# Kernel tuning notes

Hardware: AMD Instinct MI355X
Metric: run time of the kernel (lower is better)

## Reference

```python
import jax, jax.numpy as jnp
import numpy as np

HEADS = 8


def setup_inputs() -> dict:
    key = jax.random.key(0)
    k1, k2, k3, k4, k5, k6 = jax.random.split(key, 6)
    B, S, E = 2, 2048, 512
    D = E // HEADS
    return {
        "values": jax.random.normal(k1, (B, S, E), dtype=jnp.float32),
        "keys": jax.random.normal(k2, (B, S, E), dtype=jnp.float32),
        "queries": jax.random.normal(k3, (B, S, E), dtype=jnp.float32),
        "mask": jax.random.randint(k4, (B, 1, 1, S), 0, 2, dtype=jnp.int32),
        "W_v": jax.random.normal(k5, (D, D), dtype=jnp.float32) * (1.0 / np.sqrt(D)),
        "W_o": jax.random.normal(k6, (E, E), dtype=jnp.float32) * (1.0 / np.sqrt(E)),
        "b_o": jnp.zeros((E,), dtype=jnp.float32),
    }


def reference(values, keys, queries, mask, W_v, W_o, b_o):
    B, S, E = queries.shape
    H = HEADS
    D = E // H
    # reshape to (b, s, h, d) and apply the SAME W_v linear to v, k, q
    # (faithful to the original, which calls self.values on all three)
    v = jnp.einsum('bshd,ed->bshe', values.reshape(B, -1, H, D), W_v)
    k = jnp.einsum('bshd,ed->bshe', keys.reshape(B, -1, H, D), W_v)
    q = jnp.einsum('bshd,ed->bshe', queries.reshape(B, -1, H, D), W_v)
    # unscaled attention scores (original has no 1/sqrt(d))
    energy = jnp.einsum('bqhd,bkhd->bhqk', q, k)  # (b, h, q, k)
    energy = jnp.where(mask == 0, -jnp.inf, energy)
    attn = jax.nn.softmax(energy, axis=3)
    out = jnp.einsum('bhqk,bkhd->bqhd', attn, v)  # (b, q, h, d)
    out = out.reshape(B, S, E)
    return out @ W_o.T + b_o
```

## Files before the change

kernel.cpp:

```cpp
#include <hip/hip_runtime.h>


#define B_ 2
#define S_ 2048
#define E_ 512
#define H_ 8
#define D_ 64

#define LOG2E 1.4426950408889634f
#define KEEP_BIAS (-92.332483f)

typedef unsigned short ushort_t;
typedef __attribute__((ext_vector_type(8))) short short8;
typedef __attribute__((ext_vector_type(8))) _Float16 half8;
typedef __attribute__((ext_vector_type(4))) float f32x4;

__device__ __forceinline__ ushort_t f2bs(float x) {
    union { float f; unsigned int u; } a; a.f = x;
    unsigned int u = a.u;
    u += 0x7fffu + ((u >> 16) & 1u);
    return (ushort_t)(u >> 16);
}
__device__ __forceinline__ float bs2f(ushort_t h) {
    union { unsigned int u; float f; } a; a.u = ((unsigned int)h) << 16;
    return a.f;
}
__device__ __forceinline__ ushort_t f2hs(float x) {
    _Float16 h = (_Float16)x;
    ushort_t u; __builtin_memcpy(&u, &h, 2);
    return u;
}
__device__ __forceinline__ void split16(const float4* g, ushort_t* hi, ushort_t* lo) {
    #pragma unroll
    for (int q = 0; q < 4; ++q) {
        float4 f = g[q];
        float vv[4] = {f.x, f.y, f.z, f.w};
        #pragma unroll
        for (int j = 0; j < 4; ++j) {
            ushort_t h = f2bs(vv[j]);
            hi[q * 4 + j] = h;
            lo[q * 4 + j] = f2bs(vv[j] - bs2f(h));
        }
    }
}

__global__ void __launch_bounds__(256) proj_mfma(
    const float* __restrict__ quer, const float* __restrict__ keys,
    const float* __restrict__ vals, const float* __restrict__ Wv,
    const float* __restrict__ Wo,
    ushort_t* __restrict__ qf, ushort_t* __restrict__ kf,
    ushort_t* __restrict__ vt, ushort_t* __restrict__ Wob)
{
    __shared__ ushort_t Ah[64 * 72], Al[64 * 72];
    __shared__ ushort_t Bh[64 * 72], Bl[64 * 72];
    const int tens = blockIdx.y;
    const int bx = blockIdx.x;
    const int t = threadIdx.x;

    if (tens == 3) {
        if (bx < 128) {
            int g = (bx * 256 + t) * 8;
            float4 f0 = *(const float4*)(Wo + g);
            float4 f1 = *(const float4*)(Wo + g + 4);
            ushort_t tmp[8] = {f2bs(f0.x), f2bs(f0.y), f2bs(f0.z), f2bs(f0.w),
                               f2bs(f1.x), f2bs(f1.y), f2bs(f1.z), f2bs(f1.w)};
            *(uint4*)&Wob[g] = *(uint4*)tmp;
        }
        return;
    }

    const float* src = tens == 0 ? quer : (tens == 1 ? keys : vals);
    const int st = bx & 31, bh = bx >> 5;
    const int b = bh >> 3, h = bh & 7;
    const int s0 = st * 64;

    {
        int e = t >> 2, dg = (t & 3) * 16;
        ushort_t th[16], tl[16];
        split16((const float4*)(Wv + e * 64 + dg), th, tl);
        *(uint4*)&Bh[e * 72 + dg] = *(uint4*)th;  *(uint4*)&Bh[e * 72 + dg + 8] = *(uint4*)(th + 8);
        *(uint4*)&Bl[e * 72 + dg] = *(uint4*)tl;  *(uint4*)&Bl[e * 72 + dg + 8] = *(uint4*)(tl + 8);
    }
    {
        int row = t >> 2, cg = (t & 3) * 16;
        const float* g = src + ((size_t)b * S_ + s0 + row) * 512 + h * 64 + cg;
        ushort_t th[16], tl[16];
        split16((const float4*)g, th, tl);
        *(uint4*)&Ah[row * 72 + cg] = *(uint4*)th;  *(uint4*)&Ah[row * 72 + cg + 8] = *(uint4*)(th + 8);
        *(uint4*)&Al[row * 72 + cg] = *(uint4*)tl;  *(uint4*)&Al[row * 72 + cg + 8] = *(uint4*)(tl + 8);
    }
    __syncthreads();

    const int w = t >> 6, lm = t & 15, quad = (t >> 4) & 3;
    f32x4 acc[4];
    #pragma unroll
    for (int nt = 0; nt < 4; ++nt) acc[nt] = (f32x4){0.f, 0.f, 0.f, 0.f};

    __builtin_amdgcn_s_setprio(1);
    #pragma unroll
    for (int kk = 0; kk < 2; ++kk) {
        short8 ah = *(const short8*)&Ah[(w * 16 + lm) * 72 + kk * 32 + quad * 8];
        short8 al = *(const short8*)&Al[(w * 16 + lm) * 72 + kk * 32 + quad * 8];
        #pragma unroll
        for (int nt = 0; nt < 4; ++nt) {
            short8 bh8 = *(const short8*)&Bh[(nt * 16 + lm) * 72 + kk * 32 + quad * 8];
            short8 bl8 = *(const short8*)&Bl[(nt * 16 + lm) * 72 + kk * 32 + quad * 8];
            acc[nt] = __builtin_amdgcn_mfma_f32_16x16x32_bf16(ah, bh8, acc[nt], 0, 0, 0);
            acc[nt] = __builtin_amdgcn_mfma_f32_16x16x32_bf16(al, bh8, acc[nt], 0, 0, 0);
            acc[nt] = __builtin_amdgcn_mfma_f32_16x16x32_bf16(ah, bl8, acc[nt], 0, 0, 0);
        }
    }
    __builtin_amdgcn_s_setprio(0);

    if (tens < 2) {
        ushort_t* dst = tens == 0 ? qf : kf;
        const float sc = tens == 0 ? LOG2E : 1.0f;
        #pragma unroll
        for (int nt = 0; nt < 4; ++nt) {
            #pragma unroll
            for (int r = 0; r < 4; ++r) {
                size_t addr = ((size_t)bh * S_ + s0 + w * 16 + quad * 4 + r) * 64 + nt * 16 + lm;
                dst[addr] = f2hs(acc[nt][r] * sc);
            }
        }
    } else {
        #pragma unroll
        for (int nt = 0; nt < 4; ++nt) {
            unsigned int p0 = (unsigned int)f2bs(acc[nt][0]) | ((unsigned int)f2bs(acc[nt][1]) << 16);
            unsigned int p1 = (unsigned int)f2bs(acc[nt][2]) | ((unsigned int)f2bs(acc[nt][3]) << 16);
            uint2 pk; pk.x = p0; pk.y = p1;
            size_t addr = ((size_t)bh * 64 + nt * 16 + lm) * S_ + s0 + w * 16 + quad * 4;
            *(uint2*)&vt[addr] = pk;
        }
    }
}

__global__ void __launch_bounds__(512, 2) attn_mfma(
    const ushort_t* __restrict__ qf, const ushort_t* __restrict__ kf,
    const ushort_t* __restrict__ vt, const int* __restrict__ mask,
    ushort_t* __restrict__ ctx)
{
    __shared__ ushort_t Ks[4][64 * 72];
    __shared__ ushort_t Vt[4][64 * 72];
    __shared__ ushort_t Ps[8][32 * 72];
    __shared__ float    mb[4][64];

    const int bx0 = blockIdx.x;
    const int bx = (bx0 & 7) * 64 + (bx0 >> 3);
    const int qt = bx & 31;
    const int bh = bx >> 5;
    const int b  = bh >> 3;
    const int t  = threadIdx.x;
    const int w  = t >> 6;
    const int wq = w & 1;
    const int ws = w >> 1;
    const int lm = t & 15, quad = (t >> 4) & 3;
    const int lane = t & 63;
    const int q0 = qt * 64;

    const int stile = w & 3;
    const bool isV = w >= 4;
    const size_t kstage0 = ((size_t)bh * S_ + stile * 64 + lane) * 64;
    const size_t vstage0 = ((size_t)bh * 64 + lane) * S_ + stile * 64;
    ushort_t* sdst = isV ? &Vt[stile][lane * 72] : &Ks[stile][lane * 72];
    const ushort_t* sgl = isV ? vt : kf;
    const size_t sg0 = isV ? vstage0 : kstage0;
    const size_t sgstep = isV ? 256 : 16384;

    half8 aq00, aq01, aq10, aq11;
    {
        size_t qr0 = ((size_t)bh * S_ + q0 + wq * 32 + lm) * 64 + quad * 8;
        size_t qr1 = ((size_t)bh * S_ + q0 + wq * 32 + 16 + lm) * 64 + quad * 8;
        aq00 = *(const half8*)&qf[qr0];
        aq01 = *(const half8*)&qf[qr0 + 32];
        aq10 = *(const half8*)&qf[qr1];
        aq11 = *(const half8*)&qf[qr1 + 32];
    }
    short8 ones;
    #pragma unroll
    for (int j = 0; j < 8; ++j) ones[j] = (short)0x3F80;

    f32x4 acc[2][4];
    f32x4 accl[2];
    #pragma unroll
    for (int qg = 0; qg < 2; ++qg) {
        accl[qg] = (f32x4){0.f, 0.f, 0.f, 0.f};
        #pragma unroll
        for (int nt = 0; nt < 4; ++nt) acc[qg][nt] = (f32x4){0.f, 0.f, 0.f, 0.f};
    }

    {
        uint4 p0 = *(const uint4*)&sgl[sg0];
        uint4 p1 = *(const uint4*)&sgl[sg0 + 8];
        uint4 p2 = *(const uint4*)&sgl[sg0 + 16];
        uint4 p3 = *(const uint4*)&sgl[sg0 + 24];
        uint4 p4 = *(const uint4*)&sgl[sg0 + 32];
        uint4 p5 = *(const uint4*)&sgl[sg0 + 40];
        uint4 p6 = *(const uint4*)&sgl[sg0 + 48];
        uint4 p7 = *(const uint4*)&sgl[sg0 + 56];
        *(uint4*)&sdst[0]  = p0;  *(uint4*)&sdst[8]  = p1;
        *(uint4*)&sdst[16] = p2;  *(uint4*)&sdst[24] = p3;
        *(uint4*)&sdst[32] = p4;  *(uint4*)&sdst[40] = p5;
        *(uint4*)&sdst[48] = p6;  *(uint4*)&sdst[56] = p7;
        if (t < 256) mb[t >> 6][t & 63] = mask[b * S_ + t] ? KEEP_BIAS : -1e30f;
    }
    __syncthreads();

    for (int is = 0; is < 8; ++is) {
        const bool pf = is < 7;

        uint4 s0r, s1r, s2r, s3r, s4r, s5r, s6r, s7r; int mnx = 0;
        if (pf) {
            size_t g = sg0 + (size_t)(is + 1) * sgstep;
            s0r = *(const uint4*)&sgl[g];
            s1r = *(const uint4*)&sgl[g + 8];
            s2r = *(const uint4*)&sgl[g + 16];
            s3r = *(const uint4*)&sgl[g + 24];
            s4r = *(const uint4*)&sgl[g + 32];
            s5r = *(const uint4*)&sgl[g + 40];
            s6r = *(const uint4*)&sgl[g + 48];
            s7r = *(const uint4*)&sgl[g + 56];
            if (t < 256) mnx = mask[b * S_ + (is + 1) * 256 + t];
        }

        const ushort_t* Kc = Ks[ws];
        const ushort_t* Vc = Vt[ws];

        #pragma unroll
        for (int nt = 0; nt < 4; ++nt) {
            f32x4 binit = *(const f32x4*)&mb[ws][nt * 16 + quad * 4];
            f32x4 s0v = binit, s1v = binit;
            __builtin_amdgcn_s_setprio(1);
            #pragma unroll
            for (int kk = 0; kk < 2; ++kk) {
                half8 ak = *(const half8*)&Kc[(nt * 16 + lm) * 72 + kk * 32 + quad * 8];
                half8 aqa = kk ? aq01 : aq00;
                half8 aqb = kk ? aq11 : aq10;
                s0v = __builtin_amdgcn_mfma_f32_16x16x32_f16(ak, aqa, s0v, 0, 0, 0);
                s1v = __builtin_amdgcn_mfma_f32_16x16x32_f16(ak, aqb, s1v, 0, 0, 0);
            }
            __builtin_amdgcn_s_setprio(0);
            uint2 p0d, p1d;
            p0d.x = (unsigned int)f2bs(__builtin_amdgcn_exp2f(s0v[0])) |
                    ((unsigned int)f2bs(__builtin_amdgcn_exp2f(s0v[1])) << 16);
            p0d.y = (unsigned int)f2bs(__builtin_amdgcn_exp2f(s0v[2])) |
                    ((unsigned int)f2bs(__builtin_amdgcn_exp2f(s0v[3])) << 16);
            p1d.x = (unsigned int)f2bs(__builtin_amdgcn_exp2f(s1v[0])) |
                    ((unsigned int)f2bs(__builtin_amdgcn_exp2f(s1v[1])) << 16);
            p1d.y = (unsigned int)f2bs(__builtin_amdgcn_exp2f(s1v[2])) |
                    ((unsigned int)f2bs(__builtin_amdgcn_exp2f(s1v[3])) << 16);
            *(uint2*)&Ps[w][(lm) * 72 + nt * 16 + quad * 4]      = p0d;
            *(uint2*)&Ps[w][(16 + lm) * 72 + nt * 16 + quad * 4] = p1d;
        }

        __builtin_amdgcn_s_setprio(1);
        #pragma unroll
        for (int kk = 0; kk < 2; ++kk) {
            short8 ap0 = *(const short8*)&Ps[w][(lm) * 72 + kk * 32 + quad * 8];
            short8 ap1 = *(const short8*)&Ps[w][(16 + lm) * 72 + kk * 32 + quad * 8];
            #pragma unroll
            for (int nt = 0; nt < 4; ++nt) {
                short8 bv = *(const short8*)&Vc[(nt * 16 + lm) * 72 + kk * 32 + quad * 8];
                acc[0][nt] = __builtin_amdgcn_mfma_f32_16x16x32_bf16(ap0, bv, acc[0][nt], 0, 0, 0);
                acc[1][nt] = __builtin_amdgcn_mfma_f32_16x16x32_bf16(ap1, bv, acc[1][nt], 0, 0, 0);
            }
            accl[0] = __builtin_amdgcn_mfma_f32_16x16x32_bf16(ap0, ones, accl[0], 0, 0, 0);
            accl[1] = __builtin_amdgcn_mfma_f32_16x16x32_bf16(ap1, ones, accl[1], 0, 0, 0);
        }
        __builtin_amdgcn_s_setprio(0);

        __syncthreads();
        if (pf) {
            *(uint4*)&sdst[0]  = s0r;  *(uint4*)&sdst[8]  = s1r;
            *(uint4*)&sdst[16] = s2r;  *(uint4*)&sdst[24] = s3r;
            *(uint4*)&sdst[32] = s4r;  *(uint4*)&sdst[40] = s5r;
            *(uint4*)&sdst[48] = s6r;  *(uint4*)&sdst[56] = s7r;
            if (t < 256) mb[t >> 6][t & 63] = mnx ? KEEP_BIAS : -1e30f;
            __syncthreads();
        }
    }

    float* cfO = (float*)Ks;
    float* cfL = (float*)Vt;
    __syncthreads();
    if (ws & 1) {
        const int wid = wq * 2 + (ws >> 1);
        #pragma unroll
        for (int qg = 0; qg < 2; ++qg) {
            const int bO = ((wid * 2 + qg) * 64 + lane) * 17;
            #pragma unroll
            for (int nt = 0; nt < 4; ++nt)
                #pragma unroll
                for (int r = 0; r < 4; ++r) cfO[bO + nt * 4 + r] = acc[qg][nt][r];
            const int bL = ((wid * 2 + qg) * 64 + lane) * 5;
            #pragma unroll
            for (int r = 0; r < 4; ++r) cfL[bL + r] = accl[qg][r];
        }
    }
    __syncthreads();
    if (!(ws & 1)) {
        const int wid = wq * 2 + (ws >> 1);
        #pragma unroll
        for (int qg = 0; qg < 2; ++qg) {
            const int bO = ((wid * 2 + qg) * 64 + lane) * 17;
            #pragma unroll
            for (int nt = 0; nt < 4; ++nt)
                #pragma unroll
                for (int r = 0; r < 4; ++r) acc[qg][nt][r] += cfO[bO + nt * 4 + r];
            const int bL = ((wid * 2 + qg) * 64 + lane) * 5;
            #pragma unroll
            for (int r = 0; r < 4; ++r) accl[qg][r] += cfL[bL + r];
        }
    }
    __syncthreads();
    if (ws == 2) {
        #pragma unroll
        for (int qg = 0; qg < 2; ++qg) {
            const int bO = ((wq * 2 + qg) * 64 + lane) * 17;
            #pragma unroll
            for (int nt = 0; nt < 4; ++nt)
                #pragma unroll
                for (int r = 0; r < 4; ++r) cfO[bO + nt * 4 + r] = acc[qg][nt][r];
            const int bL = ((wq * 2 + qg) * 64 + lane) * 5;
            #pragma unroll
            for (int r = 0; r < 4; ++r) cfL[bL + r] = accl[qg][r];
        }
    }
    __syncthreads();
    if (ws == 0) {
        const int h = bh & 7;
        #pragma unroll
        for (int qg = 0; qg < 2; ++qg) {
            const int bO = ((wq * 2 + qg) * 64 + lane) * 17;
            const int bL = ((wq * 2 + qg) * 64 + lane) * 5;
            #pragma unroll
            for (int r = 0; r < 4; ++r) {
                float l = accl[qg][r] + cfL[bL + r];
                float inv = 1.f / l;
                int s = q0 + wq * 32 + qg * 16 + quad * 4 + r;
                #pragma unroll
                for (int nt = 0; nt < 4; ++nt) {
                    float o = acc[qg][nt][r] + cfO[bO + nt * 4 + r];
                    ctx[((size_t)b * S_ + s) * E_ + h * D_ + nt * 16 + lm] = f2bs(o * inv);
                }
            }
        }
    }
}

__global__ void __launch_bounds__(512, 4) outproj_mfma(
    const ushort_t* __restrict__ ctx, const ushort_t* __restrict__ Wob,
    const float* __restrict__ bo, float* __restrict__ out)
{
    __shared__ ushort_t sm[4][64 * 72];
    const int m0 = blockIdx.x * 64, n0 = blockIdx.y * 64;
    const int t = threadIdx.x;
    const int w = t >> 6, wq = w & 3, wk = w >> 2;
    const int lm = t & 15, quad = (t >> 4) & 3;
    const int srow = t >> 3, scg = (t & 7) * 8;

    const size_t abase = (size_t)(m0 + srow) * E_ + scg;
    const size_t bbase = (size_t)(n0 + srow) * E_ + scg;

    f32x4 acc[4];
    #pragma unroll
    for (int nt = 0; nt < 4; ++nt) acc[nt] = (f32x4){0.f, 0.f, 0.f, 0.f};

    *(uint4*)&sm[0][srow * 72 + scg] = *(const uint4*)&ctx[abase];
    *(uint4*)&sm[1][srow * 72 + scg] = *(const uint4*)&ctx[abase + 256];
    *(uint4*)&sm[2][srow * 72 + scg] = *(const uint4*)&Wob[bbase];
    *(uint4*)&sm[3][srow * 72 + scg] = *(const uint4*)&Wob[bbase + 256];
    __syncthreads();

    const ushort_t* Ac = sm[wk];
    const ushort_t* Bc = sm[2 + wk];

    for (int is = 0; is < 4; ++is) {
        const bool pf = is < 3;
        uint4 pa0, pa1, pb0, pb1;
        if (pf) {
            pa0 = *(const uint4*)&ctx[abase + (size_t)(is + 1) * 64];
            pa1 = *(const uint4*)&ctx[abase + 256 + (size_t)(is + 1) * 64];
            pb0 = *(const uint4*)&Wob[bbase + (size_t)(is + 1) * 64];
            pb1 = *(const uint4*)&Wob[bbase + 256 + (size_t)(is + 1) * 64];
        }

        __builtin_amdgcn_s_setprio(1);
        #pragma unroll
        for (int kk = 0; kk < 2; ++kk) {
            short8 a = *(const short8*)&Ac[(wq * 16 + lm) * 72 + kk * 32 + quad * 8];
            #pragma unroll
            for (int nt = 0; nt < 4; ++nt) {
                short8 bb = *(const short8*)&Bc[(nt * 16 + lm) * 72 + kk * 32 + quad * 8];
                acc[nt] = __builtin_amdgcn_mfma_f32_16x16x32_bf16(a, bb, acc[nt], 0, 0, 0);
            }
        }
        __builtin_amdgcn_s_setprio(0);

        __syncthreads();
        if (pf) {
            *(uint4*)&sm[0][srow * 72 + scg] = pa0;
            *(uint4*)&sm[1][srow * 72 + scg] = pa1;
            *(uint4*)&sm[2][srow * 72 + scg] = pb0;
            *(uint4*)&sm[3][srow * 72 + scg] = pb1;
            __syncthreads();
        }
    }

    float* cf = (float*)sm;
    const int lane = t & 63;
    if (wk == 1) {
        const int base = (wq * 64 + lane) * 18;
        #pragma unroll
        for (int nt = 0; nt < 4; ++nt) {
            #pragma unroll
            for (int r = 0; r < 4; r += 2) {
                float2 v2; v2.x = acc[nt][r]; v2.y = acc[nt][r + 1];
                *(float2*)&cf[base + nt * 4 + r] = v2;
            }
        }
    }
    __syncthreads();
    if (wk == 0) {
        const int base = (wq * 64 + lane) * 18;
        #pragma unroll
        for (int nt = 0; nt < 4; ++nt) {
            float bias = bo[n0 + nt * 16 + lm];
            #pragma unroll
            for (int r = 0; r < 4; ++r) {
                int m = m0 + wq * 16 + quad * 4 + r;
                out[(size_t)m * E_ + n0 + nt * 16 + lm] =
                    acc[nt][r] + cf[base + nt * 4 + r] + bias;
            }
        }
    }
}

extern "C" void kernel_launch(void* const* d_in, const int* in_sizes, int n_in,
                              void* d_out, int out_size, void* d_ws, size_t ws_size,
                              hipStream_t stream) {
    const float* vals = (const float*)d_in[0];
    const float* keys = (const float*)d_in[1];
    const float* quer = (const float*)d_in[2];
    const int*   mask = (const int*)d_in[3];
    const float* Wv   = (const float*)d_in[4];
    const float* Wo   = (const float*)d_in[5];
    const float* bo   = (const float*)d_in[6];
    float* out = (float*)d_out;

    const size_t N = (size_t)B_ * H_ * S_ * D_;
    ushort_t* ws  = (ushort_t*)d_ws;
    ushort_t* qf  = ws;
    ushort_t* kf  = ws + N;
    ushort_t* vt  = ws + 2 * N;
    ushort_t* ctx = ws + 3 * N;
    ushort_t* Wob = ws + 4 * N;

    proj_mfma<<<dim3(B_ * H_ * (S_ / 64), 4), 256, 0, stream>>>(
        quer, keys, vals, Wv, Wo, qf, kf, vt, Wob);
    attn_mfma<<<B_ * H_ * (S_ / 64), 512, 0, stream>>>(qf, kf, vt, mask, ctx);
    outproj_mfma<<<dim3((B_ * S_) / 64, E_ / 64), 512, 0, stream>>>(ctx, Wob, bo, out);
}
```

Before: 145.5 us.

## Halve attention block to four waves splitting keys two ways

The attention kernel drops from 8 waves to 4 per block. The key dimension is now split across 2 wave groups instead of 4, with 16 stages of 128 keys in place of 8 stages of 256, and shared buffers shrink to match. The cross-wave reduction of partial outputs and row sums becomes a single exchange step instead of a two-level tree. This cuts reduction overhead and shared memory per block, which could allow more resident blocks. The cost is more loop iterations and barriers per block and less parallelism within each block.

```diff
diff --git a/kernel.cpp b/kernel.cpp
--- a/kernel.cpp
+++ b/kernel.cpp
@@ -135,15 +135,15 @@
     }
 }
 
-__global__ void __launch_bounds__(512, 2) attn_mfma(
+__global__ void __launch_bounds__(256, 2) attn_mfma(
     const ushort_t* __restrict__ qf, const ushort_t* __restrict__ kf,
     const ushort_t* __restrict__ vt, const int* __restrict__ mask,
     ushort_t* __restrict__ ctx)
 {
-    __shared__ ushort_t Ks[4][64 * 72];
-    __shared__ ushort_t Vt[4][64 * 72];
-    __shared__ ushort_t Ps[8][32 * 72];
-    __shared__ float    mb[4][64];
+    __shared__ ushort_t Ks[2][64 * 72];
+    __shared__ ushort_t Vt[2][64 * 72];
+    __shared__ ushort_t Ps[4][32 * 72];
+    __shared__ float    mb[2][64];
 
     const int bx0 = blockIdx.x;
     const int bx = (bx0 & 7) * 64 + (bx0 >> 3);
@@ -158,14 +158,14 @@
     const int lane = t & 63;
     const int q0 = qt * 64;
 
-    const int stile = w & 3;
-    const bool isV = w >= 4;
-    const size_t kstage0 = ((size_t)bh * S_ + stile * 64 + lane) * 64;
-    const size_t vstage0 = ((size_t)bh * 64 + lane) * S_ + stile * 64;
-    ushort_t* sdst = isV ? &Vt[stile][lane * 72] : &Ks[stile][lane * 72];
+    const int stW = w & 1;
+    const bool isV = w >= 2;
+    const size_t kst0 = ((size_t)bh * S_ + stW * 64 + lane) * 64;
+    const size_t vst0 = ((size_t)bh * 64 + lane) * S_ + stW * 64;
+    ushort_t* sdst = isV ? &Vt[stW][lane * 72] : &Ks[stW][lane * 72];
     const ushort_t* sgl = isV ? vt : kf;
-    const size_t sg0 = isV ? vstage0 : kstage0;
-    const size_t sgstep = isV ? 256 : 16384;
+    const size_t sg0 = isV ? vst0 : kst0;
+    const size_t sgstep = isV ? 128 : 8192;
 
     half8 aq00, aq01, aq10, aq11;
     {
@@ -202,12 +202,12 @@
         *(uint4*)&sdst[16] = p2;  *(uint4*)&sdst[24] = p3;
         *(uint4*)&sdst[32] = p4;  *(uint4*)&sdst[40] = p5;
         *(uint4*)&sdst[48] = p6;  *(uint4*)&sdst[56] = p7;
-        if (t < 256) mb[t >> 6][t & 63] = mask[b * S_ + t] ? KEEP_BIAS : -1e30f;
-    }
-    __syncthreads();
-
-    for (int is = 0; is < 8; ++is) {
-        const bool pf = is < 7;
+        if (t < 128) mb[t >> 6][t & 63] = mask[b * S_ + t] ? KEEP_BIAS : -1e30f;
+    }
+    __syncthreads();
+
+    for (int is = 0; is < 16; ++is) {
+        const bool pf = is < 15;
 
         uint4 s0r, s1r, s2r, s3r, s4r, s5r, s6r, s7r; int mnx = 0;
         if (pf) {
@@ -220,7 +220,7 @@
             s5r = *(const uint4*)&sgl[g + 40];
             s6r = *(const uint4*)&sgl[g + 48];
             s7r = *(const uint4*)&sgl[g + 56];
-            if (t < 256) mnx = mask[b * S_ + (is + 1) * 256 + t];
+            if (t < 128) mnx = mask[b * S_ + (is + 1) * 128 + t];
         }
 
         const ushort_t* Kc = Ks[ws];
@@ -275,7 +275,7 @@
             *(uint4*)&sdst[16] = s2r;  *(uint4*)&sdst[24] = s3r;
             *(uint4*)&sdst[32] = s4r;  *(uint4*)&sdst[40] = s5r;
             *(uint4*)&sdst[48] = s6r;  *(uint4*)&sdst[56] = s7r;
-            if (t < 256) mb[t >> 6][t & 63] = mnx ? KEEP_BIAS : -1e30f;
+            if (t < 128) mb[t >> 6][t & 63] = mnx ? KEEP_BIAS : -1e30f;
             __syncthreads();
         }
     }
@@ -283,45 +283,16 @@
     float* cfO = (float*)Ks;
     float* cfL = (float*)Vt;
     __syncthreads();
-    if (ws & 1) {
-        const int wid = wq * 2 + (ws >> 1);
+    if (ws == 1) {
         #pragma unroll
         for (int qg = 0; qg < 2; ++qg) {
-            const int bO = ((wid * 2 + qg) * 64 + lane) * 17;
+            const int sid = wq * 2 + qg;
+            const int bO = (sid * 64 + lane) * 17;
+            const int bL = (sid * 64 + lane) * 5;
             #pragma unroll
             for (int nt = 0; nt < 4; ++nt)
                 #pragma unroll
                 for (int r = 0; r < 4; ++r) cfO[bO + nt * 4 + r] = acc[qg][nt][r];
-            const int bL = ((wid * 2 + qg) * 64 + lane) * 5;
-            #pragma unroll
-            for (int r = 0; r < 4; ++r) cfL[bL + r] = accl[qg][r];
-        }
-    }
-    __syncthreads();
-    if (!(ws & 1)) {
-        const int wid = wq * 2 + (ws >> 1);
-        #pragma unroll
-        for (int qg = 0; qg < 2; ++qg) {
-            const int bO = ((wid * 2 + qg) * 64 + lane) * 17;
-            #pragma unroll
-            for (int nt = 0; nt < 4; ++nt)
-                #pragma unroll
-                for (int r = 0; r < 4; ++r) acc[qg][nt][r] += cfO[bO + nt * 4 + r];
-            const int bL = ((wid * 2 + qg) * 64 + lane) * 5;
-            #pragma unroll
-            for (int r = 0; r < 4; ++r) accl[qg][r] += cfL[bL + r];
-        }
-    }
-    __syncthreads();
-    if (ws == 2) {
-        #pragma unroll
-        for (int qg = 0; qg < 2; ++qg) {
-            const int bO = ((wq * 2 + qg) * 64 + lane) * 17;
-            #pragma unroll
-            for (int nt = 0; nt < 4; ++nt)
-                #pragma unroll
-                for (int r = 0; r < 4; ++r) cfO[bO + nt * 4 + r] = acc[qg][nt][r];
-            const int bL = ((wq * 2 + qg) * 64 + lane) * 5;
             #pragma unroll
             for (int r = 0; r < 4; ++r) cfL[bL + r] = accl[qg][r];
         }
@@ -331,8 +302,9 @@
         const int h = bh & 7;
         #pragma unroll
         for (int qg = 0; qg < 2; ++qg) {
-            const int bO = ((wq * 2 + qg) * 64 + lane) * 17;
-            const int bL = ((wq * 2 + qg) * 64 + lane) * 5;
+            const int sid = wq * 2 + qg;
+            const int bO = (sid * 64 + lane) * 17;
+            const int bL = (sid * 64 + lane) * 5;
             #pragma unroll
             for (int r = 0; r < 4; ++r) {
                 float l = accl[qg][r] + cfL[bL + r];
@@ -458,6 +430,6 @@
 
     proj_mfma<<<dim3(B_ * H_ * (S_ / 64), 4), 256, 0, stream>>>(
         quer, keys, vals, Wv, Wo, qf, kf, vt, Wob);
-    attn_mfma<<<B_ * H_ * (S_ / 64), 512, 0, stream>>>(qf, kf, vt, mask, ctx);
+    attn_mfma<<<B_ * H_ * (S_ / 64), 256, 0, stream>>>(qf, kf, vt, mask, ctx);
     outproj_mfma<<<dim3((B_ * S_) / 64, E_ / 64), 512, 0, stream>>>(ctx, Wob, bo, out);
 }
```

After: 139.0 us. 1.05x faster.
